# Kernel tuning notes

Hardware: AMD Instinct MI355X
Metric: run time of the kernel (lower is better)

## Reference

```python
import jax, jax.numpy as jnp
import numpy as np

SIGMA = 1.0          # influence distance of kernel points
KERNEL_RADIUS = 1.0  # radius within which kernel points live


def setup_inputs() -> dict:
    key = jax.random.key(0)
    k0, k1, k2, k3, k4 = jax.random.split(key, 5)
    B, M, K_NB, D_IN, D_OUT, K_PTS = 4, 16384, 32, 64, 64, 15
    X = jax.random.normal(k0, (B, M, 3), dtype=jnp.float32)          # point coords
    F = jax.random.normal(k1, (B, M, D_IN), dtype=jnp.float32)        # point features
    N = jax.random.randint(k2, (B, M, K_NB), 0, M)                    # neighbor indices
    Q = jax.random.uniform(k3, (K_PTS, 3), minval=-KERNEL_RADIUS,
                           maxval=KERNEL_RADIUS, dtype=jnp.float32)   # kernel points
    W = jax.random.normal(k4, (K_PTS, D_IN, D_OUT), dtype=jnp.float32) * 0.05
    return {"X": X, "F": F, "N": N, "Q": Q, "W": W}


def reference(X, F, N, Q, W):
    # Gather neighbor coordinates and features: [B, M, k, 3] / [B, M, k, d_in]
    gather = jax.vmap(lambda a, idx: a[idx])
    Xn = gather(X, N)
    Fn = gather(F, N)
    # Relative neighbor positions w.r.t. each center point
    r = Xn - X[:, :, None, :]                                  # [B, M, k, 3]
    # Distance of each relative position to each kernel point
    d = jnp.linalg.norm(r[:, :, :, None, :] - Q, axis=-1)      # [B, M, k, Kp]
    # Linear correlation influence (KPConv)
    h = jnp.maximum(0.0, 1.0 - d / SIGMA)                      # [B, M, k, Kp]
    # Distance-weighted neighbor aggregation per kernel point
    Fk = jnp.einsum('bmkp,bmkd->bmpd', h, Fn)                  # [B, M, Kp, d_in]
    # Per-kernel-point linear maps, summed over kernel points
    return jnp.einsum('bmpd,pde->bme', Fk, W)                  # [B, M, d_out]
```

## Files before the change

kernel.cpp:

```cpp
#include <hip/hip_runtime.h>
#include <hip/hip_bf16.h>


#define BATCH 4
#define MPTS  16384
#define KNB   32
#define DIN   64
#define DOUT  64
#define KP    15
#define K2P   1024
#define KSTEPS (K2P/32)
#define ROWB  (K2P*2)
#define PTS   (BATCH*MPTS)
#define PPB   32
#define NBLK  (PTS/PPB)
#define WBELEMS (K2P*DOUT)
#define WBBLK (WBELEMS/256)
#define FBBLK (PTS*DIN/8/256)

typedef __bf16 bf16x8 __attribute__((ext_vector_type(8)));
typedef float  f32x4  __attribute__((ext_vector_type(4)));
typedef unsigned short u16x8 __attribute__((ext_vector_type(8)));

static __device__ __forceinline__ unsigned short f2b(float x) {
    __bf16 h = (__bf16)x;
    return __builtin_bit_cast(unsigned short, h);
}

__global__ void prep_all(const float* __restrict__ W, const float* __restrict__ F,
                         unsigned short* __restrict__ wb, unsigned short* __restrict__ fb) {
    int bid = blockIdx.x;
    if (bid < WBBLK) {
        int idx = bid * 256 + threadIdx.x;
        int i    = idx & 7;
        int lane = (idx >> 3) & 63;
        int ks   = (idx >> 9) & 31;
        int et   = idx >> 14;
        int kap  = ks * 32 + ((lane >> 4) << 3) + i;
        int n = kap >> 6;
        int g = (kap >> 4) & 3;
        int t = (kap >> 2) & 3;
        int r = kap & 3;
        int p = g * 4 + r;
        int d = n * 4 + t;
        int e = et * 16 + (lane & 15);
        float v = (p < KP) ? W[(p * DIN + d) * DOUT + e] : 0.f;
        wb[idx] = f2b(v);
    } else {
        int i = (bid - WBBLK) * 256 + threadIdx.x;
        const float4* s = reinterpret_cast<const float4*>(F) + (size_t)i * 2;
        float4 a = s[0], b = s[1];
        u16x8 o;
        o[0] = f2b(a.x); o[1] = f2b(a.y); o[2] = f2b(a.z); o[3] = f2b(a.w);
        o[4] = f2b(b.x); o[5] = f2b(b.y); o[6] = f2b(b.z); o[7] = f2b(b.w);
        *(reinterpret_cast<u16x8*>(fb) + i) = o;
    }
}

__global__ __launch_bounds__(256, 2)
void kpconv_main(const float* __restrict__ X, const unsigned short* __restrict__ FB,
                 const int* __restrict__ NB, const float* __restrict__ Q,
                 const unsigned short* __restrict__ WB, float* __restrict__ OUT) {
    __shared__ unsigned short fk[PPB * K2P];
    char* const fkb = reinterpret_cast<char*>(fk);

    const int tid  = threadIdx.x;
    const int wv   = tid >> 6;
    const int lane = tid & 63;
    const int g16  = lane >> 4;
    const int r16  = lane & 15;

    float qx = 1.0e3f, qy = 0.f, qz = 0.f;
    if (r16 < KP) { qx = Q[r16 * 3 + 0]; qy = Q[r16 * 3 + 1]; qz = Q[r16 * 3 + 2]; }
    const float qq   = qx * qx + qy * qy + qz * qz;
    const float nq2x = -2.f * qx, nq2y = -2.f * qy, nq2z = -2.f * qz;

    const int bid     = blockIdx.x;
    const int base_pt = (bid & 7) * (PTS / 8) + (bid >> 3) * PPB;
    const int boff    = (base_pt >> 14) * MPTS;
    const int pid0    = base_pt + wv * 8;

    #pragma unroll
    for (int e = 0; e < 4; ++e) {
        int ent = lane + e * 64;
        int j = ent >> 5, k = ent & 31;
        int pid = pid0 + j;
        int nb  = NB[(size_t)pid * KNB + k];
        int gidx = boff + nb;
        const float* xn = X + (size_t)gidx * 3;
        const float* xc = X + (size_t)pid * 3;
        float rx = xn[0] - xc[0];
        float ry = xn[1] - xc[1];
        float rz = xn[2] - xc[2];
        float rr = fmaf(rx, rx, fmaf(ry, ry, rz * rz));
        int slot = (k & 24) | ((k ^ (k >> 3)) & 7);
        *reinterpret_cast<float4*>(fkb + (wv * 8 + j) * ROWB + slot * 16) =
            make_float4(rx, ry, rz, rr);
    }

    union U { uint2 d; unsigned short s[4]; };
    U L[4][8];

    auto issue_gather = [&](int pid_j, U* Lj) {
        const int* nbp = NB + (size_t)pid_j * KNB + g16 * 8;
        int4 a = *reinterpret_cast<const int4*>(nbp);
        int4 b = *reinterpret_cast<const int4*>(nbp + 4);
        int g[8] = {a.x, a.y, a.z, a.w, b.x, b.y, b.z, b.w};
        #pragma unroll
        for (int i = 0; i < 8; ++i)
            Lj[i].d = *reinterpret_cast<const uint2*>(
                FB + ((size_t)(boff + g[i]) << 6) + (r16 << 2));
    };

    issue_gather(pid0 + 0, L[0]);
    issue_gather(pid0 + 1, L[1]);
    issue_gather(pid0 + 2, L[2]);
    issue_gather(pid0 + 3, L[3]);

    #pragma unroll
    for (int j = 0; j < 8; ++j) {
        const int row = wv * 8 + j;

        bf16x8 ah;
        #pragma unroll
        for (int i = 0; i < 8; ++i) {
            float4 rv = *reinterpret_cast<const float4*>(
                fkb + row * ROWB + (g16 * 8 + (i ^ g16)) * 16);
            float d2 = fmaf(rv.x, nq2x, fmaf(rv.y, nq2y, fmaf(rv.z, nq2z, rv.w + qq)));
            d2 = fmaxf(d2, 0.f);
            ah[i] = (__bf16)fmaxf(1.f - __builtin_amdgcn_sqrtf(d2), 0.f);
        }

        bf16x8 bfr[4];
        #pragma unroll
        for (int t = 0; t < 4; ++t)
            #pragma unroll
            for (int i = 0; i < 8; ++i)
                bfr[t][i] = __builtin_bit_cast(__bf16, L[j & 3][i].s[t]);

        if (j < 4) issue_gather(pid0 + j + 4, L[j & 3]);

        const f32x4 z = {0.f, 0.f, 0.f, 0.f};
        f32x4 accs[4];
        #pragma unroll
        for (int t = 0; t < 4; ++t)
            accs[t] = __builtin_amdgcn_mfma_f32_16x16x32_bf16(ah, bfr[t], z, 0, 0, 0);

        bf16x8 w0, w1;
        #pragma unroll
        for (int r = 0; r < 4; ++r) {
            w0[r]     = (__bf16)accs[0][r];
            w0[4 + r] = (__bf16)accs[1][r];
            w1[r]     = (__bf16)accs[2][r];
            w1[4 + r] = (__bf16)accs[3][r];
        }
        int swz  = (row & 7) ^ (r16 & 7);
        int off0 = row * ROWB + (r16 * 8 + ((g16 * 2 + 0) ^ swz)) * 16;
        int off1 = row * ROWB + (r16 * 8 + ((g16 * 2 + 1) ^ swz)) * 16;
        *reinterpret_cast<bf16x8*>(fkb + off0) = w0;
        *reinterpret_cast<bf16x8*>(fkb + off1) = w1;
    }

    __syncthreads();

    const unsigned short* wbp = WB + ((size_t)(wv * KSTEPS) * 64 + lane) * 8;
    asm volatile("" : "+v"(wbp));

    f32x4 o0 = {0.f, 0.f, 0.f, 0.f};
    f32x4 o1 = {0.f, 0.f, 0.f, 0.f};
    #pragma unroll
    for (int ks = 0; ks < KSTEPS; ++ks) {
        bf16x8 b = *reinterpret_cast<const bf16x8*>(wbp + ks * 512);
        int stored = (ks * 4 + g16) ^ (r16 & 7) ^ ((ks >> 1) & 7);
        bf16x8 a0 = *reinterpret_cast<const bf16x8*>(fkb + r16 * ROWB + stored * 16);
        bf16x8 a1 = *reinterpret_cast<const bf16x8*>(fkb + (16 + r16) * ROWB + stored * 16);
        o0 = __builtin_amdgcn_mfma_f32_16x16x32_bf16(a0, b, o0, 0, 0, 0);
        o1 = __builtin_amdgcn_mfma_f32_16x16x32_bf16(a1, b, o1, 0, 0, 0);
    }

    #pragma unroll
    for (int r = 0; r < 4; ++r) {
        int p0 = base_pt + g16 * 4 + r;
        OUT[(size_t)p0 * DOUT + wv * 16 + r16] = o0[r];
        int p1 = base_pt + 16 + g16 * 4 + r;
        OUT[(size_t)p1 * DOUT + wv * 16 + r16] = o1[r];
    }
}

extern "C" void kernel_launch(void* const* d_in, const int* in_sizes, int n_in,
                              void* d_out, int out_size, void* d_ws, size_t ws_size,
                              hipStream_t stream) {
    const float* X = (const float*)d_in[0];
    const float* F = (const float*)d_in[1];
    const int*   N = (const int*)d_in[2];
    const float* Q = (const float*)d_in[3];
    const float* W = (const float*)d_in[4];
    float* OUT = (float*)d_out;
    unsigned short* WB = (unsigned short*)d_ws;
    unsigned short* FB = WB + WBELEMS;

    prep_all<<<WBBLK + FBBLK, 256, 0, stream>>>(W, F, WB, FB);
    kpconv_main<<<NBLK, 256, 0, stream>>>(X, FB, N, Q, WB, OUT);
}
```

Baseline: 58.59 us.

## Pad coordinates to float4, cache neighbor indices in LDS, shrink gather pipeline

The prep kernel now also writes the point coordinates padded to float4 in the workspace, so the main kernel fetches each neighbor position with one 16-byte load instead of three scalar loads. Global neighbor indices (with the batch offset already added) are stored in shared memory, so the feature gathers read them from LDS instead of reloading them from global memory. The register prefetch depth drops from four points to two, which frees registers but leaves less latency hiding. The padded path runs only when the workspace is large enough; otherwise the old coordinate path is used.

```diff
diff --git a/kernel.cpp b/kernel.cpp
--- a/kernel.cpp
+++ b/kernel.cpp
@@ -17,6 +17,10 @@
 #define WBELEMS (K2P*DOUT)
 #define WBBLK (WBELEMS/256)
 #define FBBLK (PTS*DIN/8/256)
+#define XPBLK (PTS/256)
+#define FBOFF 131072
+#define XPOFF (FBOFF + PTS*DIN*2)
+#define WSNEED (XPOFF + PTS*16)
 
 typedef __bf16 bf16x8 __attribute__((ext_vector_type(8)));
 typedef float  f32x4  __attribute__((ext_vector_type(4)));
@@ -28,7 +32,9 @@
 }
 
 __global__ void prep_all(const float* __restrict__ W, const float* __restrict__ F,
-                         unsigned short* __restrict__ wb, unsigned short* __restrict__ fb) {
+                         const float* __restrict__ X,
+                         unsigned short* __restrict__ wb, unsigned short* __restrict__ fb,
+                         float4* __restrict__ xp, int do_xp) {
     int bid = blockIdx.x;
     if (bid < WBBLK) {
         int idx = bid * 256 + threadIdx.x;
@@ -46,7 +52,7 @@
         int e = et * 16 + (lane & 15);
         float v = (p < KP) ? W[(p * DIN + d) * DOUT + e] : 0.f;
         wb[idx] = f2b(v);
-    } else {
+    } else if (bid < WBBLK + FBBLK) {
         int i = (bid - WBBLK) * 256 + threadIdx.x;
         const float4* s = reinterpret_cast<const float4*>(F) + (size_t)i * 2;
         float4 a = s[0], b = s[1];
@@ -54,14 +60,21 @@
         o[0] = f2b(a.x); o[1] = f2b(a.y); o[2] = f2b(a.z); o[3] = f2b(a.w);
         o[4] = f2b(b.x); o[5] = f2b(b.y); o[6] = f2b(b.z); o[7] = f2b(b.w);
         *(reinterpret_cast<u16x8*>(fb) + i) = o;
-    }
-}
-
+    } else if (do_xp) {
+        int row = (bid - WBBLK - FBBLK) * 256 + threadIdx.x;
+        const float* x = X + (size_t)row * 3;
+        xp[row] = make_float4(x[0], x[1], x[2], 0.f);
+    }
+}
+
+template<bool UXP>
 __global__ __launch_bounds__(256, 2)
-void kpconv_main(const float* __restrict__ X, const unsigned short* __restrict__ FB,
+void kpconv_main(const float* __restrict__ X, const float4* __restrict__ XP,
+                 const unsigned short* __restrict__ FB,
                  const int* __restrict__ NB, const float* __restrict__ Q,
                  const unsigned short* __restrict__ WB, float* __restrict__ OUT) {
     __shared__ unsigned short fk[PPB * K2P];
+    __shared__ int idxs[4][8][KNB];
     char* const fkb = reinterpret_cast<char*>(fk);
 
     const int tid  = threadIdx.x;
@@ -87,35 +100,39 @@
         int pid = pid0 + j;
         int nb  = NB[(size_t)pid * KNB + k];
         int gidx = boff + nb;
-        const float* xn = X + (size_t)gidx * 3;
-        const float* xc = X + (size_t)pid * 3;
-        float rx = xn[0] - xc[0];
-        float ry = xn[1] - xc[1];
-        float rz = xn[2] - xc[2];
+        float rx, ry, rz;
+        if constexpr (UXP) {
+            float4 xn = XP[gidx];
+            float4 xc = XP[pid];
+            rx = xn.x - xc.x; ry = xn.y - xc.y; rz = xn.z - xc.z;
+        } else {
+            const float* xn = X + (size_t)gidx * 3;
+            const float* xc = X + (size_t)pid * 3;
+            rx = xn[0] - xc[0]; ry = xn[1] - xc[1]; rz = xn[2] - xc[2];
+        }
         float rr = fmaf(rx, rx, fmaf(ry, ry, rz * rz));
         int slot = (k & 24) | ((k ^ (k >> 3)) & 7);
         *reinterpret_cast<float4*>(fkb + (wv * 8 + j) * ROWB + slot * 16) =
             make_float4(rx, ry, rz, rr);
+        idxs[wv][j][k] = gidx;
     }
 
     union U { uint2 d; unsigned short s[4]; };
-    U L[4][8];
-
-    auto issue_gather = [&](int pid_j, U* Lj) {
-        const int* nbp = NB + (size_t)pid_j * KNB + g16 * 8;
-        int4 a = *reinterpret_cast<const int4*>(nbp);
-        int4 b = *reinterpret_cast<const int4*>(nbp + 4);
+    U L[2][8];
+
+    auto issue_gather = [&](int j, U* Lj) {
+        const int4* ip = reinterpret_cast<const int4*>(&idxs[wv][j][g16 * 8]);
+        int4 a = ip[0];
+        int4 b = ip[1];
         int g[8] = {a.x, a.y, a.z, a.w, b.x, b.y, b.z, b.w};
         #pragma unroll
         for (int i = 0; i < 8; ++i)
             Lj[i].d = *reinterpret_cast<const uint2*>(
-                FB + ((size_t)(boff + g[i]) << 6) + (r16 << 2));
+                FB + ((size_t)g[i] << 6) + (r16 << 2));
     };
 
-    issue_gather(pid0 + 0, L[0]);
-    issue_gather(pid0 + 1, L[1]);
-    issue_gather(pid0 + 2, L[2]);
-    issue_gather(pid0 + 3, L[3]);
+    issue_gather(0, L[0]);
+    issue_gather(1, L[1]);
 
     #pragma unroll
     for (int j = 0; j < 8; ++j) {
@@ -136,9 +153,9 @@
         for (int t = 0; t < 4; ++t)
             #pragma unroll
             for (int i = 0; i < 8; ++i)
-                bfr[t][i] = __builtin_bit_cast(__bf16, L[j & 3][i].s[t]);
-
-        if (j < 4) issue_gather(pid0 + j + 4, L[j & 3]);
+                bfr[t][i] = __builtin_bit_cast(__bf16, L[j & 1][i].s[t]);
+
+        if (j < 6) issue_gather(j + 2, L[j & 1]);
 
         const f32x4 z = {0.f, 0.f, 0.f, 0.f};
         f32x4 accs[4];
@@ -197,8 +214,16 @@
     const float* W = (const float*)d_in[4];
     float* OUT = (float*)d_out;
     unsigned short* WB = (unsigned short*)d_ws;
-    unsigned short* FB = WB + WBELEMS;
-
-    prep_all<<<WBBLK + FBBLK, 256, 0, stream>>>(W, F, WB, FB);
-    kpconv_main<<<NBLK, 256, 0, stream>>>(X, FB, N, Q, WB, OUT);
-}
+    unsigned short* FB = (unsigned short*)((char*)d_ws + FBOFF);
+    float4*         XP = (float4*)((char*)d_ws + XPOFF);
+
+    const int use_xp = (ws_size >= (size_t)WSNEED) ? 1 : 0;
+
+    prep_all<<<WBBLK + FBBLK + (use_xp ? XPBLK : 0), 256, 0, stream>>>(
+        W, F, X, WB, FB, XP, use_xp);
+
+    if (use_xp)
+        kpconv_main<true><<<NBLK, 256, 0, stream>>>(X, XP, FB, N, Q, WB, OUT);
+    else
+        kpconv_main<false><<<NBLK, 256, 0, stream>>>(X, XP, FB, N, Q, WB, OUT);
+}
```

Result: faster. 55.07 us (median of 2 runs) (-6.0%).
